# Kernel tuning notes

Measured on AMD Instinct MI355X. Metric: run time of the kernel, lower is better.

## Reference

```python
import jax, jax.numpy as jnp
import numpy as np

N, IN_DIM, OUT_DIM, H = 8192, 512, 512, 1
BN_EPS = 1e-5


def _lin(key, fan_in, fan_out):
    k1, k2 = jax.random.split(key)
    b = 1.0 / np.sqrt(fan_in)
    W = jax.random.uniform(k1, (fan_in, fan_out), jnp.float32, -b, b)
    bias = jax.random.uniform(k2, (fan_out,), jnp.float32, -b, b)
    return W, bias


def setup_inputs() -> dict:
    key = jax.random.key(0)
    ks = jax.random.split(key, 12)
    h = jax.random.normal(ks[0], (N, IN_DIM), jnp.float32)
    A = (jax.random.uniform(ks[1], (N, N)) < 0.01).astype(jnp.float32)
    qw, qb = _lin(ks[2], IN_DIM, OUT_DIM * H)
    kw, kb = _lin(ks[3], IN_DIM, OUT_DIM * H)
    vw, vb = _lin(ks[4], IN_DIM, OUT_DIM * H)
    ow, ob = _lin(ks[5], OUT_DIM, OUT_DIM)
    f1w, f1b = _lin(ks[6], OUT_DIM, OUT_DIM * 2)
    f2w, f2b = _lin(ks[7], OUT_DIM * 2, OUT_DIM)
    bn1_g = jax.random.normal(ks[8], (OUT_DIM,)) * 0.1 + 1.0
    bn1_b = jax.random.normal(ks[9], (OUT_DIM,)) * 0.1
    bn1_m = jax.random.normal(ks[10], (OUT_DIM,)) * 0.1
    bn1_v = jax.random.uniform(ks[11], (OUT_DIM,), jnp.float32, 0.5, 1.5)
    ks2 = jax.random.split(jax.random.fold_in(key, 7), 4)
    bn2_g = jax.random.normal(ks2[0], (OUT_DIM,)) * 0.1 + 1.0
    bn2_b = jax.random.normal(ks2[1], (OUT_DIM,)) * 0.1
    bn2_m = jax.random.normal(ks2[2], (OUT_DIM,)) * 0.1
    bn2_v = jax.random.uniform(ks2[3], (OUT_DIM,), jnp.float32, 0.5, 1.5)
    return dict(A=A, h=h, qw=qw, qb=qb, kw=kw, kb=kb, vw=vw, vb=vb,
                ow=ow, ob=ob, f1w=f1w, f1b=f1b, f2w=f2w, f2b=f2b,
                bn1_g=bn1_g, bn1_b=bn1_b, bn1_m=bn1_m, bn1_v=bn1_v,
                bn2_g=bn2_g, bn2_b=bn2_b, bn2_m=bn2_m, bn2_v=bn2_v)


def _bn_eval(x, g, b, m, v):
    return (x - m) * jax.lax.rsqrt(v + BN_EPS) * g + b


def reference(A, h, qw, qb, kw, kb, vw, vb, ow, ob, f1w, f1b, f2w, f2b,
              bn1_g, bn1_b, bn1_m, bn1_v, bn2_g, bn2_b, bn2_m, bn2_v):
    n = h.shape[0]
    scaling = OUT_DIM ** (-0.5)
    # q/k/v: [N, D, H] as in torch reshape of [N, D*H]
    q = (h @ qw + qb).reshape(n, OUT_DIM, H) * scaling
    k = (h @ kw + kb).reshape(n, OUT_DIM, H)
    v = (h @ vw + vb).reshape(n, OUT_DIM, H)
    qh = jnp.transpose(q, (2, 0, 1))          # (H, N, D)
    kh = jnp.transpose(k, (2, 1, 0))          # (H, D, N)
    vh = jnp.transpose(v, (2, 0, 1))          # (H, N, D)
    attn = jnp.einsum('hnd,hdm->hnm', qh, kh) * A[None]   # (H, N, N)
    attn = jax.nn.softmax(attn, axis=0)        # NOTE: softmax over HEAD axis, as in source
    out = jnp.einsum('hnm,hmd->hnd', attn, vh).reshape(n, H * OUT_DIM)
    # GTLayer (eval mode: dropout = identity, BN uses running stats)
    x = out @ ow + ob
    x = x + h                                  # residual
    x = _bn_eval(x, bn1_g, bn1_b, bn1_m, bn1_v)
    h2 = x
    f = jax.nn.relu(x @ f1w + f1b) @ f2w + f2b
    x = h2 + f
    x = _bn_eval(x, bn2_g, bn2_b, bn2_m, bn2_v)
    return x
```

## Files before the change

### kernel.cpp

```cpp
#include <hip/hip_runtime.h>

#define NROWS 8192
#define DIM 512
#define HID 1024
#define BN_EPS 1e-5f

typedef unsigned short ushort_t;
typedef __attribute__((ext_vector_type(8))) __bf16 bf16x8;
typedef __attribute__((ext_vector_type(4))) float f32x4;

union U4 {
    uint4 u;
    bf16x8 b;
    ushort_t s[8];
};

static __device__ __forceinline__ float b2f(ushort_t u) {
    union { float f; unsigned int i; } c;
    c.i = ((unsigned int)u) << 16;
    return c.f;
}

static __device__ __forceinline__ ushort_t f2b(float f) {
    union { float f; unsigned int i; } c;
    c.f = f;
    unsigned int i = c.i;
    unsigned int r = (i + 0x7FFFu + ((i >> 16) & 1u)) >> 16;
    return (ushort_t)r;
}

__global__ void prep_kernel(const float* __restrict__ h, float* __restrict__ hs,
                            ushort_t* __restrict__ hB,
                            const float* __restrict__ f1w,
                            const float* __restrict__ g1, const float* __restrict__ v1,
                            const float* __restrict__ f2w,
                            ushort_t* __restrict__ W1T, ushort_t* __restrict__ W2T) {
    __shared__ float tile[32][33];
    int bid = blockIdx.x;
    if (bid < 256) {
        int t = threadIdx.x;
        int col0 = (t & 127) * 4;
        int rsub = t >> 7;
        int row0 = bid * 32;
        float acc[4] = {0.f, 0.f, 0.f, 0.f};
        for (int r = 0; r < 16; ++r) {
            int row = row0 + r * 2 + rsub;
            float4 v = *(const float4*)(h + (size_t)row * DIM + col0);
            acc[0] += v.x; acc[1] += v.y; acc[2] += v.z; acc[3] += v.w;
            ushort_t bv[4];
            bv[0] = f2b(v.x); bv[1] = f2b(v.y); bv[2] = f2b(v.z); bv[3] = f2b(v.w);
            *(uint2*)(hB + (size_t)row * DIM + col0) = *(uint2*)bv;
        }
#pragma unroll
        for (int j = 0; j < 4; ++j) atomicAdd(&hs[col0 + j], acc[j]);
    } else if (bid < 768) {
        int b = bid - 256;
        int tx = threadIdx.x & 31, ty = threadIdx.x >> 5;
        int bx = (b & 31) * 32, by = (b >> 5) * 32;
#pragma unroll
        for (int i = 0; i < 32; i += 8)
            tile[ty + i][tx] = f1w[(size_t)(by + ty + i) * HID + bx + tx];
        __syncthreads();
        int r = by + tx;
        float a1 = g1[r] * rsqrtf(v1[r] + BN_EPS);
#pragma unroll
        for (int i = 0; i < 32; i += 8)
            W1T[(size_t)(bx + ty + i) * DIM + r] = f2b(tile[tx][ty + i] * a1);
    } else {
        int b2 = bid - 768;
        int tx = threadIdx.x & 31, ty = threadIdx.x >> 5;
        int bx = (b2 & 15) * 32, by = (b2 >> 4) * 32;
#pragma unroll
        for (int i = 0; i < 32; i += 8)
            tile[ty + i][tx] = f2w[(size_t)(by + ty + i) * DIM + bx + tx];
        __syncthreads();
#pragma unroll
        for (int i = 0; i < 32; i += 8)
            W2T[(size_t)(bx + ty + i) * HID + by + tx] = f2b(tile[tx][ty + i]);
    }
}

__global__ void matvec_kernel(const float* __restrict__ xin, const float* __restrict__ W,
                              const float* __restrict__ bvec, float scaleB,
                              float* __restrict__ outv, int ncols) {
    __shared__ float red[8][32];
    int t = threadIdx.x;
    int col = blockIdx.x * 32 + (t & 31);
    int ks = t >> 5;
    float s = 0.f;
    for (int ki = 0; ki < 64; ++ki) {
        int k = ks * 64 + ki;
        s += xin[k] * W[(size_t)k * ncols + col];
    }
    red[ks][t & 31] = s;
    __syncthreads();
    if (ks == 0) {
        float tot = scaleB * bvec[col];
#pragma unroll
        for (int r = 0; r < 8; ++r) tot += red[r][t & 31];
        outv[col] = tot;
    }
}

__global__ void matvec_b1p_kernel(const float* __restrict__ tvec,
                                  const float* __restrict__ g1, const float* __restrict__ b1,
                                  const float* __restrict__ m1, const float* __restrict__ v1,
                                  const float* __restrict__ W, const float* __restrict__ bvec,
                                  float* __restrict__ outv) {
    __shared__ float red[8][32];
    int t = threadIdx.x;
    int col = blockIdx.x * 32 + (t & 31);
    int ks = t >> 5;
    float s = 0.f;
    for (int ki = 0; ki < 64; ++ki) {
        int k = ks * 64 + ki;
        float a1 = g1[k] * rsqrtf(v1[k] + BN_EPS);
        float q0 = tvec[k] * a1 + (b1[k] - m1[k] * a1);
        s += q0 * W[(size_t)k * HID + col];
    }
    red[ks][t & 31] = s;
    __syncthreads();
    if (ks == 0) {
        float tot = bvec[col];
#pragma unroll
        for (int r = 0; r < 8; ++r) tot += red[r][t & 31];
        outv[col] = tot;
    }
}

__global__ __launch_bounds__(256) void gemm1_kernel(const ushort_t* __restrict__ A,
                                                    const ushort_t* __restrict__ BT,
                                                    const float* __restrict__ bias,
                                                    ushort_t* __restrict__ C) {
    const int K = DIM, Nn = HID, LDA = 72;
    __shared__ ushort_t As[128 * LDA];
    __shared__ ushort_t Bs[128 * LDA];
    int tid = threadIdx.x;
    int lane = tid & 63, w = tid >> 6;
    int wm = (w & 1) * 64, wn = (w >> 1) * 64;
    int bm = blockIdx.y * 128, bn = blockIdx.x * 128;

    f32x4 acc[4][4] = {};

    int r0 = tid >> 2, kc0 = (tid & 3) * 8;
    int r1 = r0 + 64;

    for (int k0 = 0; k0 < K; k0 += 64) {
        __syncthreads();
        uint4 a00 = *(const uint4*)(A + (size_t)(bm + r0) * K + k0 + kc0);
        uint4 a01 = *(const uint4*)(A + (size_t)(bm + r0) * K + k0 + kc0 + 32);
        uint4 a10 = *(const uint4*)(A + (size_t)(bm + r1) * K + k0 + kc0);
        uint4 a11 = *(const uint4*)(A + (size_t)(bm + r1) * K + k0 + kc0 + 32);
        uint4 b00 = *(const uint4*)(BT + (size_t)(bn + r0) * K + k0 + kc0);
        uint4 b01 = *(const uint4*)(BT + (size_t)(bn + r0) * K + k0 + kc0 + 32);
        uint4 b10 = *(const uint4*)(BT + (size_t)(bn + r1) * K + k0 + kc0);
        uint4 b11 = *(const uint4*)(BT + (size_t)(bn + r1) * K + k0 + kc0 + 32);
        *(uint4*)(As + r0 * LDA + kc0) = a00;
        *(uint4*)(As + r0 * LDA + kc0 + 32) = a01;
        *(uint4*)(As + r1 * LDA + kc0) = a10;
        *(uint4*)(As + r1 * LDA + kc0 + 32) = a11;
        *(uint4*)(Bs + r0 * LDA + kc0) = b00;
        *(uint4*)(Bs + r0 * LDA + kc0 + 32) = b01;
        *(uint4*)(Bs + r1 * LDA + kc0) = b10;
        *(uint4*)(Bs + r1 * LDA + kc0 + 32) = b11;
        __syncthreads();

#pragma unroll
        for (int s = 0; s < 2; ++s) {
            int koff = (lane >> 4) * 8 + s * 32;
            bf16x8 af[4], bfr[4];
#pragma unroll
            for (int i = 0; i < 4; ++i) {
                U4 t;
                t.u = *(const uint4*)(As + (wm + i * 16 + (lane & 15)) * LDA + koff);
                af[i] = t.b;
            }
#pragma unroll
            for (int j = 0; j < 4; ++j) {
                U4 t;
                t.u = *(const uint4*)(Bs + (wn + j * 16 + (lane & 15)) * LDA + koff);
                bfr[j] = t.b;
            }
#pragma unroll
            for (int i = 0; i < 4; ++i)
#pragma unroll
                for (int j = 0; j < 4; ++j)
                    acc[i][j] = __builtin_amdgcn_mfma_f32_16x16x32_bf16(af[i], bfr[j], acc[i][j], 0, 0, 0);
        }
    }

#pragma unroll
    for (int i = 0; i < 4; ++i) {
        int row0 = bm + wm + i * 16 + (lane >> 4) * 4;
#pragma unroll
        for (int j = 0; j < 4; ++j) {
            int col = bn + wn + j * 16 + (lane & 15);
            float bv = bias[col];
#pragma unroll
            for (int r = 0; r < 4; ++r) {
                float v = fmaxf(acc[i][j][r] + bv, 0.f);
                C[(size_t)(row0 + r) * Nn + col] = f2b(v);
            }
        }
    }
}

__global__ __launch_bounds__(256) void gemm2_kernel(const ushort_t* __restrict__ A,
                                                    const ushort_t* __restrict__ BT,
                                                    const float* __restrict__ bias,
                                                    const ushort_t* __restrict__ hB,
                                                    const float* __restrict__ tvec,
                                                    const float* __restrict__ g1,
                                                    const float* __restrict__ b1,
                                                    const float* __restrict__ m1,
                                                    const float* __restrict__ v1,
                                                    const float* __restrict__ g2,
                                                    const float* __restrict__ b2,
                                                    const float* __restrict__ m2,
                                                    const float* __restrict__ v2,
                                                    float* __restrict__ out) {
    const int K = HID, LDA = 72;
    __shared__ ushort_t As[128 * LDA];
    __shared__ ushort_t Bs[64 * LDA];
    int tid = threadIdx.x;
    int lane = tid & 63, w = tid >> 6;
    int wm = (w & 1) * 64, wn = (w >> 1) * 32;
    int bm = blockIdx.y * 128, bn = blockIdx.x * 64;

    f32x4 acc[4][2] = {};

    int r0 = tid >> 2, kc0 = (tid & 3) * 8;
    int r1 = r0 + 64;

    for (int k0 = 0; k0 < K; k0 += 64) {
        __syncthreads();
        uint4 a00 = *(const uint4*)(A + (size_t)(bm + r0) * K + k0 + kc0);
        uint4 a01 = *(const uint4*)(A + (size_t)(bm + r0) * K + k0 + kc0 + 32);
        uint4 a10 = *(const uint4*)(A + (size_t)(bm + r1) * K + k0 + kc0);
        uint4 a11 = *(const uint4*)(A + (size_t)(bm + r1) * K + k0 + kc0 + 32);
        uint4 b00 = *(const uint4*)(BT + (size_t)(bn + r0) * K + k0 + kc0);
        uint4 b01 = *(const uint4*)(BT + (size_t)(bn + r0) * K + k0 + kc0 + 32);
        *(uint4*)(As + r0 * LDA + kc0) = a00;
        *(uint4*)(As + r0 * LDA + kc0 + 32) = a01;
        *(uint4*)(As + r1 * LDA + kc0) = a10;
        *(uint4*)(As + r1 * LDA + kc0 + 32) = a11;
        *(uint4*)(Bs + r0 * LDA + kc0) = b00;
        *(uint4*)(Bs + r0 * LDA + kc0 + 32) = b01;
        __syncthreads();

#pragma unroll
        for (int s = 0; s < 2; ++s) {
            int koff = (lane >> 4) * 8 + s * 32;
            bf16x8 af[4], bfr[2];
#pragma unroll
            for (int i = 0; i < 4; ++i) {
                U4 t;
                t.u = *(const uint4*)(As + (wm + i * 16 + (lane & 15)) * LDA + koff);
                af[i] = t.b;
            }
#pragma unroll
            for (int j = 0; j < 2; ++j) {
                U4 t;
                t.u = *(const uint4*)(Bs + (wn + j * 16 + (lane & 15)) * LDA + koff);
                bfr[j] = t.b;
            }
#pragma unroll
            for (int i = 0; i < 4; ++i)
#pragma unroll
                for (int j = 0; j < 2; ++j)
                    acc[i][j] = __builtin_amdgcn_mfma_f32_16x16x32_bf16(af[i], bfr[j], acc[i][j], 0, 0, 0);
        }
    }

#pragma unroll
    for (int i = 0; i < 4; ++i) {
        int row0 = bm + wm + i * 16 + (lane >> 4) * 4;
#pragma unroll
        for (int j = 0; j < 2; ++j) {
            int col = bn + wn + j * 16 + (lane & 15);
            float a1c = g1[col] * rsqrtf(v1[col] + BN_EPS);
            float q0c = tvec[col] * a1c + (b1[col] - m1[col] * a1c);
            float a2c = g2[col] * rsqrtf(v2[col] + BN_EPS);
            float c2c = b2[col] - m2[col] * a2c;
            float bv = bias[col];
#pragma unroll
            for (int r = 0; r < 4; ++r) {
                int row = row0 + r;
                float x1 = b2f(hB[(size_t)row * DIM + col]) * a1c + q0c;
                out[(size_t)row * DIM + col] = (x1 + acc[i][j][r] + bv) * a2c + c2c;
            }
        }
    }
}

extern "C" void kernel_launch(void* const* d_in, const int* in_sizes, int n_in,
                              void* d_out, int out_size, void* d_ws, size_t ws_size,
                              hipStream_t stream) {
    const float* h = (const float*)d_in[1];
    const float* vw = (const float*)d_in[6];
    const float* vb = (const float*)d_in[7];
    const float* ow = (const float*)d_in[8];
    const float* ob = (const float*)d_in[9];
    const float* f1w = (const float*)d_in[10];
    const float* f1b = (const float*)d_in[11];
    const float* f2w = (const float*)d_in[12];
    const float* fb2 = (const float*)d_in[13];
    const float* g1 = (const float*)d_in[14];
    const float* b1 = (const float*)d_in[15];
    const float* m1 = (const float*)d_in[16];
    const float* v1 = (const float*)d_in[17];
    const float* g2 = (const float*)d_in[18];
    const float* b2 = (const float*)d_in[19];
    const float* m2 = (const float*)d_in[20];
    const float* v2 = (const float*)d_in[21];
    float* out = (float*)d_out;

    char* ws = (char*)d_ws;
    float* hs = (float*)(ws + 0);
    float* sBuf = (float*)(ws + 4096);
    float* tBuf = (float*)(ws + 8192);
    float* b1P = (float*)(ws + 16384);
    ushort_t* W1T = (ushort_t*)(ws + 32768);
    ushort_t* W2T = (ushort_t*)(ws + 32768 + 1048576);
    ushort_t* Z = (ushort_t*)(ws + 32768 + 2097152);
    ushort_t* hB = (ushort_t*)(ws + 32768 + 2097152 + 16777216);

    hipMemsetAsync(hs, 0, 512 * sizeof(float), stream);
    prep_kernel<<<1280, 256, 0, stream>>>(h, hs, hB, f1w, g1, v1, f2w, W1T, W2T);
    matvec_kernel<<<16, 256, 0, stream>>>(hs, vw, vb, 8192.0f, sBuf, 512);
    matvec_kernel<<<16, 256, 0, stream>>>(sBuf, ow, ob, 1.0f, tBuf, 512);
    matvec_b1p_kernel<<<32, 256, 0, stream>>>(tBuf, g1, b1, m1, v1, f1w, f1b, b1P);
    gemm1_kernel<<<dim3(8, 64), 256, 0, stream>>>(hB, W1T, b1P, Z);
    gemm2_kernel<<<dim3(8, 64), 256, 0, stream>>>(Z, W2T, fb2, hB, tBuf,
                                                  g1, b1, m1, v1, g2, b2, m2, v2, out);
}
```

Before: 460.4 us.

## Replace atomic column sums with partials and fuse matvec chain kernels

After: 561.0 us. 1.22x slower.

```diff
diff --git a/kernel.cpp b/kernel.cpp
--- a/kernel.cpp
+++ b/kernel.cpp
@@ -29,7 +29,7 @@
     return (ushort_t)r;
 }
 
-__global__ void prep_kernel(const float* __restrict__ h, float* __restrict__ hs,
+__global__ void prep_kernel(const float* __restrict__ h, float* __restrict__ hs_part,
                             ushort_t* __restrict__ hB,
                             const float* __restrict__ f1w,
                             const float* __restrict__ g1, const float* __restrict__ v1,
@@ -51,8 +51,15 @@
             bv[0] = f2b(v.x); bv[1] = f2b(v.y); bv[2] = f2b(v.z); bv[3] = f2b(v.w);
             *(uint2*)(hB + (size_t)row * DIM + col0) = *(uint2*)bv;
         }
-#pragma unroll
-        for (int j = 0; j < 4; ++j) atomicAdd(&hs[col0 + j], acc[j]);
+        __shared__ float part[2][512];
+#pragma unroll
+        for (int j = 0; j < 4; ++j) part[rsub][col0 + j] = acc[j];
+        __syncthreads();
+        if (rsub == 0) {
+#pragma unroll
+            for (int j = 0; j < 4; ++j)
+                hs_part[(size_t)bid * 512 + col0 + j] = part[0][col0 + j] + part[1][col0 + j];
+        }
     } else if (bid < 768) {
         int b = bid - 256;
         int tx = threadIdx.x & 31, ty = threadIdx.x >> 5;
@@ -80,51 +87,65 @@
     }
 }
 
-__global__ void matvec_kernel(const float* __restrict__ xin, const float* __restrict__ W,
-                              const float* __restrict__ bvec, float scaleB,
-                              float* __restrict__ outv, int ncols) {
+__global__ void chain_kernel(const float* __restrict__ hs_part,
+                             const float* __restrict__ vw, const float* __restrict__ vb,
+                             const float* __restrict__ ow, const float* __restrict__ ob,
+                             const float* __restrict__ f1w, const float* __restrict__ f1b,
+                             const float* __restrict__ g1, const float* __restrict__ b1,
+                             const float* __restrict__ m1, const float* __restrict__ v1,
+                             float* __restrict__ b1P) {
+    __shared__ float sh[512];
     __shared__ float red[8][32];
     int t = threadIdx.x;
+#pragma unroll
+    for (int i = 0; i < 2; ++i) {
+        int c = t + i * 256;
+        float a = 0.f;
+        for (int r = 0; r < 256; ++r) a += hs_part[(size_t)r * 512 + c];
+        sh[c] = a;
+    }
+    __syncthreads();
+    float sv[2];
+#pragma unroll
+    for (int i = 0; i < 2; ++i) {
+        int c = t + i * 256;
+        float a = 8192.0f * vb[c];
+        for (int k = 0; k < 512; ++k) a += sh[k] * vw[(size_t)k * 512 + c];
+        sv[i] = a;
+    }
+    __syncthreads();
+    sh[t] = sv[0]; sh[t + 256] = sv[1];
+    __syncthreads();
+    float tv[2];
+#pragma unroll
+    for (int i = 0; i < 2; ++i) {
+        int c = t + i * 256;
+        float a = ob[c];
+        for (int k = 0; k < 512; ++k) a += sh[k] * ow[(size_t)k * 512 + c];
+        tv[i] = a;
+    }
+    __syncthreads();
+#pragma unroll
+    for (int i = 0; i < 2; ++i) {
+        int c = t + i * 256;
+        float a1 = g1[c] * rsqrtf(v1[c] + BN_EPS);
+        sh[c] = tv[i] * a1 + (b1[c] - m1[c] * a1);
+    }
+    __syncthreads();
     int col = blockIdx.x * 32 + (t & 31);
     int ks = t >> 5;
-    float s = 0.f;
+    float acc = 0.f;
     for (int ki = 0; ki < 64; ++ki) {
         int k = ks * 64 + ki;
-        s += xin[k] * W[(size_t)k * ncols + col];
-    }
-    red[ks][t & 31] = s;
+        acc += sh[k] * f1w[(size_t)k * HID + col];
+    }
+    red[ks][t & 31] = acc;
     __syncthreads();
     if (ks == 0) {
-        float tot = scaleB * bvec[col];
+        float tot = f1b[col];
 #pragma unroll
         for (int r = 0; r < 8; ++r) tot += red[r][t & 31];
-        outv[col] = tot;
-    }
-}
-
-__global__ void matvec_b1p_kernel(const float* __restrict__ tvec,
-                                  const float* __restrict__ g1, const float* __restrict__ b1,
-                                  const float* __restrict__ m1, const float* __restrict__ v1,
-                                  const float* __restrict__ W, const float* __restrict__ bvec,
-                                  float* __restrict__ outv) {
-    __shared__ float red[8][32];
-    int t = threadIdx.x;
-    int col = blockIdx.x * 32 + (t & 31);
-    int ks = t >> 5;
-    float s = 0.f;
-    for (int ki = 0; ki < 64; ++ki) {
-        int k = ks * 64 + ki;
-        float a1 = g1[k] * rsqrtf(v1[k] + BN_EPS);
-        float q0 = tvec[k] * a1 + (b1[k] - m1[k] * a1);
-        s += q0 * W[(size_t)k * HID + col];
-    }
-    red[ks][t & 31] = s;
-    __syncthreads();
-    if (ks == 0) {
-        float tot = bvec[col];
-#pragma unroll
-        for (int r = 0; r < 8; ++r) tot += red[r][t & 31];
-        outv[col] = tot;
+        b1P[col] = tot;
     }
 }
 
@@ -293,6 +314,40 @@
     }
 }
 
+__global__ void chain_tvec_kernel(const float* __restrict__ hs_part,
+                                  const float* __restrict__ vw, const float* __restrict__ vb,
+                                  const float* __restrict__ ow, const float* __restrict__ ob,
+                                  float* __restrict__ tvec) {
+    __shared__ float sh[512];
+    int t = threadIdx.x;
+#pragma unroll
+    for (int i = 0; i < 2; ++i) {
+        int c = t + i * 256;
+        float a = 0.f;
+        for (int r = 0; r < 256; ++r) a += hs_part[(size_t)r * 512 + c];
+        sh[c] = a;
+    }
+    __syncthreads();
+    float sv[2];
+#pragma unroll
+    for (int i = 0; i < 2; ++i) {
+        int c = t + i * 256;
+        float a = 8192.0f * vb[c];
+        for (int k = 0; k < 512; ++k) a += sh[k] * vw[(size_t)k * 512 + c];
+        sv[i] = a;
+    }
+    __syncthreads();
+    sh[t] = sv[0]; sh[t + 256] = sv[1];
+    __syncthreads();
+#pragma unroll
+    for (int i = 0; i < 2; ++i) {
+        int c = t + i * 256;
+        float a = ob[c];
+        for (int k = 0; k < 512; ++k) a += sh[k] * ow[(size_t)k * 512 + c];
+        tvec[c] = a;
+    }
+}
+
 extern "C" void kernel_launch(void* const* d_in, const int* in_sizes, int n_in,
                               void* d_out, int out_size, void* d_ws, size_t ws_size,
                               hipStream_t stream) {
@@ -316,20 +371,18 @@
     float* out = (float*)d_out;
 
     char* ws = (char*)d_ws;
-    float* hs = (float*)(ws + 0);
-    float* sBuf = (float*)(ws + 4096);
-    float* tBuf = (float*)(ws + 8192);
-    float* b1P = (float*)(ws + 16384);
-    ushort_t* W1T = (ushort_t*)(ws + 32768);
-    ushort_t* W2T = (ushort_t*)(ws + 32768 + 1048576);
-    ushort_t* Z = (ushort_t*)(ws + 32768 + 2097152);
-    ushort_t* hB = (ushort_t*)(ws + 32768 + 2097152 + 16777216);
-
-    hipMemsetAsync(hs, 0, 512 * sizeof(float), stream);
-    prep_kernel<<<1280, 256, 0, stream>>>(h, hs, hB, f1w, g1, v1, f2w, W1T, W2T);
-    matvec_kernel<<<16, 256, 0, stream>>>(hs, vw, vb, 8192.0f, sBuf, 512);
-    matvec_kernel<<<16, 256, 0, stream>>>(sBuf, ow, ob, 1.0f, tBuf, 512);
-    matvec_b1p_kernel<<<32, 256, 0, stream>>>(tBuf, g1, b1, m1, v1, f1w, f1b, b1P);
+    float* hs_part = (float*)(ws + 0);
+    float* tBuf = (float*)(ws + 524288);
+    float* b1P = (float*)(ws + 528384);
+    ushort_t* W1T = (ushort_t*)(ws + 540672);
+    ushort_t* W2T = (ushort_t*)(ws + 540672 + 1048576);
+    ushort_t* Z = (ushort_t*)(ws + 540672 + 2097152);
+    ushort_t* hB = (ushort_t*)(ws + 540672 + 2097152 + 16777216);
+
+    prep_kernel<<<1280, 256, 0, stream>>>(h, hs_part, hB, f1w, g1, v1, f2w, W1T, W2T);
+    chain_tvec_kernel<<<1, 256, 0, stream>>>(hs_part, vw, vb, ow, ob, tBuf);
+    chain_kernel<<<32, 256, 0, stream>>>(hs_part, vw, vb, ow, ob, f1w, f1b,
+                                         g1, b1, m1, v1, b1P);
     gemm1_kernel<<<dim3(8, 64), 256, 0, stream>>>(hB, W1T, b1P, Z);
     gemm2_kernel<<<dim3(8, 64), 256, 0, stream>>>(Z, W2T, fb2, hB, tBuf,
                                                   g1, b1, m1, v1, g2, b2, m2, v2, out);
```
